# Kernel tuning notes

Measured on AMD Instinct MI355X. Metric: run time of the kernel, lower is better.

Reference implementation:

```python
import jax, jax.numpy as jnp
import numpy as np

N_NODES = 200000
N_EDGES = 800000
N_GRAPHS = 4096
IN_FEAT = 64
CONV_SIZES = [128, 128, 256, 256]
MAX_DEGREE = 5  # buckets 0..5 (degree clamped)
N_CLASSES = 2


def setup_inputs() -> dict:
    key = jax.random.key(0)
    ks = jax.random.split(key, 32)
    inp = {}
    inp["x"] = jax.random.normal(ks[0], (N_NODES, IN_FEAT), dtype=jnp.float32)
    inp["edge_index"] = jax.random.randint(ks[1], (2, N_EDGES), 0, N_NODES, dtype=jnp.int32)
    inp["batch"] = jnp.sort(jax.random.randint(ks[2], (N_NODES,), 0, N_GRAPHS, dtype=jnp.int32))
    # per-layer MFConv params: Wl (neighbor-sum branch, with bias), Wr (root branch, no bias),
    # one linear per degree bucket -> leading dim MAX_DEGREE+1
    c_in = IN_FEAT
    k = 3
    for li, c_out in enumerate(CONV_SIZES):
        s = 1.0 / np.sqrt(c_in)
        inp[f"Wl{li}"] = jax.random.normal(ks[k], (MAX_DEGREE + 1, c_in, c_out), dtype=jnp.float32) * s; k += 1
        inp[f"bl{li}"] = jax.random.normal(ks[k], (MAX_DEGREE + 1, c_out), dtype=jnp.float32) * 0.01; k += 1
        inp[f"Wr{li}"] = jax.random.normal(ks[k], (MAX_DEGREE + 1, c_in, c_out), dtype=jnp.float32) * s; k += 1
        c_in = c_out
    in_final = sum(CONV_SIZES) + CONV_SIZES[-1]  # concat of all layer outputs + pooled last layer
    inp["Wf"] = jax.random.normal(ks[k], (in_final, N_CLASSES), dtype=jnp.float32) * (1.0 / np.sqrt(in_final)); k += 1
    inp["bf"] = jax.random.normal(ks[k], (N_CLASSES,), dtype=jnp.float32) * 0.01
    return inp


def _mfconv(x, src, dst, deg, Wl, bl, Wr):
    # neighbor sum aggregation (source_to_target flow): msg_i = sum_{j->i} x_j
    msg = jax.ops.segment_sum(x[src], dst, num_segments=x.shape[0])  # [N, c_in]
    out = jnp.zeros((x.shape[0], Wl.shape[2]), dtype=x.dtype)
    for d in range(Wl.shape[0]):  # small fixed loop over degree buckets
        r = msg @ Wl[d] + bl[d] + x @ Wr[d]
        out = jnp.where((deg == d)[:, None], r, out)
    return out


def reference(x, edge_index, batch,
              Wl0, bl0, Wr0, Wl1, bl1, Wr1, Wl2, bl2, Wr2, Wl3, bl3, Wr3,
              Wf, bf):
    src, dst = edge_index[0], edge_index[1]
    n = x.shape[0]
    deg = jnp.clip(jnp.zeros((n,), jnp.int32).at[dst].add(1), 0, MAX_DEGREE)
    hs = []
    h = x
    for Wl, bl, Wr in ((Wl0, bl0, Wr0), (Wl1, bl1, Wr1), (Wl2, bl2, Wr2), (Wl3, bl3, Wr3)):
        h = _mfconv(h, src, dst, deg, Wl, bl, Wr)
        hs.append(h)
    # global_add_pool then repeat_interleave back to nodes == gather pooled by batch id
    h_pool = jax.ops.segment_sum(h, batch, num_segments=N_GRAPHS)  # [G, c_last]
    h_pool_ = h_pool[batch]  # [N, c_last]
    h_cat = jnp.concatenate(hs + [h_pool_], axis=1)  # [N, sum(sizes)+c_last]
    logits = h_cat @ Wf + bf
    return jax.nn.softmax(logits, axis=1)
```

## Files before the change

kernel.cpp:

```cpp
#include <hip/hip_runtime.h>
#include <cstdint>
#include <cstddef>

namespace {

constexpr int NN   = 200000;
constexpr int NE   = 800000;
constexpr int NG   = 4096;
constexpr int MAXD = 5;

constexpr int BM = 64;
constexpr int NBC = (NN + 255) / 256;
constexpr int NBLK  = (NN + BM - 1) / BM + 6;
constexpr int PERMN = NBLK * BM;

typedef _Float16 half8 __attribute__((ext_vector_type(8)));
typedef _Float16 half4 __attribute__((ext_vector_type(4)));
typedef float    f32x4 __attribute__((ext_vector_type(4)));

constexpr size_t P_L0 = (size_t)6 * 128 * 128;
constexpr size_t P_L1 = (size_t)6 * 256 * 128;
constexpr size_t P_L2 = (size_t)6 * 256 * 256;
constexpr size_t P_L3 = (size_t)6 * 512 * 256;
constexpr size_t O_P0 = 0;
constexpr size_t O_P1 = O_P0 + P_L0;
constexpr size_t O_P2 = O_P1 + P_L1;
constexpr size_t O_P3 = O_P2 + P_L2;
constexpr size_t WTOT = O_P3 + P_L3;


__global__ void k_memset32(int* __restrict__ p, int v, int n) {
    int i = blockIdx.x * 256 + threadIdx.x;
    if (i < n) p[i] = v;
}

__global__ void k_report(float* __restrict__ outp, float v, int n) {
    int i = blockIdx.x * 256 + threadIdx.x;
    if (i < n) outp[i] = v;
}

template <int CIN, int COUT>
__global__ void k_wpack(const float* __restrict__ Wl, const float* __restrict__ Wr,
                        _Float16* __restrict__ hi, _Float16* __restrict__ lo) {
    constexpr int NT = CIN / 16;
    constexpr int NB = COUT / 16;
    const int total = 6 * NT * NB * 64;
    int idx = blockIdx.x * 256 + threadIdx.x;
    if (idx >= total) return;
    const int lane = idx & 63;
    int rest = idx >> 6;
    const int nb = rest % NB; rest /= NB;
    const int ti = rest % NT;
    const int d  = rest / NT;
    const int k0 = ti * 32 + ((lane >> 4) * 8);
    const int n  = nb * 16 + (lane & 15);
    half8 hv, lv;
#pragma unroll
    for (int j = 0; j < 8; j++) {
        const int kk = k0 + j;
        const float v = (kk < CIN)
                            ? Wl[((size_t)d * CIN + kk) * COUT + n]
                            : Wr[((size_t)d * CIN + (kk - CIN)) * COUT + n];
        const _Float16 h = (_Float16)v;
        hv[j] = h;
        lv[j] = (_Float16)(v - (float)h);
    }
    *(half8*)(hi + (size_t)idx * 8) = hv;
    *(half8*)(lo + (size_t)idx * 8) = lv;
}


__global__ void k_count_deg(const int* __restrict__ dst, int* __restrict__ deg) {
    int e = blockIdx.x * 256 + threadIdx.x;
    if (e < NE) atomicAdd(&deg[dst[e]], 1);
}

__global__ void k_scan_part(const int* __restrict__ deg, int* __restrict__ part) {
    __shared__ int s[256];
    int t = threadIdx.x, i = blockIdx.x * 256 + t;
    s[t] = (i < NN) ? deg[i] : 0;
    __syncthreads();
    for (int st = 128; st > 0; st >>= 1) {
        if (t < st) s[t] += s[t + st];
        __syncthreads();
    }
    if (t == 0) part[blockIdx.x] = s[0];
}

__global__ void k_scan_single(int* __restrict__ part, int nb) {
    __shared__ int s[1024];
    int t = threadIdx.x;
    int v0 = (t < nb) ? part[t] : 0;
    s[t] = v0;
    __syncthreads();
    for (int off = 1; off < 1024; off <<= 1) {
        int v = (t >= off) ? s[t - off] : 0;
        __syncthreads();
        s[t] += v;
        __syncthreads();
    }
    if (t < nb) part[t] = s[t] - v0;
}

__global__ void k_scan_final(const int* __restrict__ deg, const int* __restrict__ part,
                             int* __restrict__ row_ptr, int* __restrict__ cursor) {
    __shared__ int s[256];
    int t = threadIdx.x, i = blockIdx.x * 256 + t;
    int v0 = (i < NN) ? deg[i] : 0;
    s[t] = v0;
    __syncthreads();
    for (int off = 1; off < 256; off <<= 1) {
        int v = (t >= off) ? s[t - off] : 0;
        __syncthreads();
        s[t] += v;
        __syncthreads();
    }
    if (i < NN) {
        int excl = s[t] - v0 + part[blockIdx.x];
        row_ptr[i] = excl;
        cursor[i]  = excl;
        if (i == NN - 1) row_ptr[NN] = excl + v0;
    }
}

__global__ void k_fill_csr(const int* __restrict__ src, const int* __restrict__ dst,
                           int* __restrict__ cursor, int* __restrict__ col) {
    int e = blockIdx.x * 256 + threadIdx.x;
    if (e < NE) {
        int d = dst[e];
        int slot = atomicAdd(&cursor[d], 1);
        col[slot] = src[e];
    }
}


__global__ void k_bucket_blockcount(const int* __restrict__ deg, int* __restrict__ blkcnt) {
    __shared__ int h[6];
    int t = threadIdx.x;
    if (t < 6) h[t] = 0;
    __syncthreads();
    int i = blockIdx.x * 256 + t;
    if (i < NN) atomicAdd(&h[min(deg[i], MAXD)], 1);
    __syncthreads();
    if (t < 6) blkcnt[t * NBC + blockIdx.x] = h[t];
}

__global__ void k_bucket_scanall(int* __restrict__ blkcnt, int* __restrict__ bpad) {
    __shared__ int tot[6];
    int t = threadIdx.x;
    if (t < 6) {
        int run = 0;
        for (int j = 0; j < NBC; j++) {
            int v = blkcnt[t * NBC + j];
            blkcnt[t * NBC + j] = run;
            run += v;
        }
        tot[t] = run;
    }
    __syncthreads();
    if (t == 0) {
        int off = 0;
        for (int b = 0; b < 6; b++) {
            bpad[b] = off;
            off += ((tot[b] + BM - 1) / BM) * BM;
        }
        bpad[6] = off;
    }
}

__global__ void k_scatter2(const int* __restrict__ deg, const int* __restrict__ blkcnt,
                           const int* __restrict__ bpad, int* __restrict__ perm) {
    __shared__ int base[6];
    int t = threadIdx.x;
    if (t < 6) base[t] = bpad[t] + blkcnt[t * NBC + blockIdx.x];
    __syncthreads();
    int i = blockIdx.x * 256 + t;
    if (i < NN) {
        int b = min(deg[i], MAXD);
        int pos = atomicAdd(&base[b], 1);
        perm[pos] = i;
    }
}


__global__ void k_aggregate128(const float* __restrict__ hin, const int* __restrict__ row_ptr,
                               const int* __restrict__ col, float* __restrict__ msg) {
    int node = blockIdx.x * 4 + (threadIdx.x >> 6);
    int lane = threadIdx.x & 63;
    int s = row_ptr[node], e = row_ptr[node + 1];
    float2 acc = make_float2(0.f, 0.f);
    int p = s;
    for (; p + 4 <= e; p += 4) {
        const int c0 = col[p], c1 = col[p + 1], c2 = col[p + 2], c3 = col[p + 3];
        const float2 v0 = *(const float2*)(hin + (size_t)c0 * 128 + lane * 2);
        const float2 v1 = *(const float2*)(hin + (size_t)c1 * 128 + lane * 2);
        const float2 v2 = *(const float2*)(hin + (size_t)c2 * 128 + lane * 2);
        const float2 v3 = *(const float2*)(hin + (size_t)c3 * 128 + lane * 2);
        acc.x += (v0.x + v1.x) + (v2.x + v3.x);
        acc.y += (v0.y + v1.y) + (v2.y + v3.y);
    }
    for (; p < e; p++) {
        const float2 v = *(const float2*)(hin + (size_t)col[p] * 128 + lane * 2);
        acc.x += v.x; acc.y += v.y;
    }
    *(float2*)(msg + (size_t)node * 128 + lane * 2) = acc;
}

template <int C0, int C1, int COUT, int MINW, bool POOL_FUSE>
__launch_bounds__(512, MINW)
__global__ void k_transform(const float* __restrict__ hin0, const float* __restrict__ hin1,
                            const int* __restrict__ row_ptr, const int* __restrict__ col,
                            const _Float16* __restrict__ wph, const _Float16* __restrict__ wpl,
                            const float* __restrict__ bias, const float* __restrict__ Wf,
                            const int* __restrict__ perm, const int* __restrict__ deg,
                            const int* __restrict__ batch,
                            float* __restrict__ out0, float* __restrict__ pool,
                            float* __restrict__ logits, int wf_off) {
    constexpr int CIN = C0 + C1;
    constexpr int NW  = CIN / 32;
    constexpr int NT  = 2 * NW;
    constexpr int NB  = COUT / 16;
    constexpr int NTN = NB / 8;
    constexpr int CPT = CIN / 8;
    constexpr int UQ  = CPT / 4;
    constexpr int PB_R = POOL_FUSE ? 64 : 1;
    constexpr int PB_C = 257;

    struct FragBuf {
        _Float16 Ah[NW][4][64][8];
        _Float16 Al[NW][4][64][8];
    };
    union SMemU {
        FragBuf f;
        float pbuf[PB_R][PB_C];
    };
    __shared__ SMemU sm;
    __shared__ int rowid[BM];
    __shared__ int gb[BM];
    __shared__ float lsx[BM], lsy[BM];

    const int t  = threadIdx.x;
    const int m0 = blockIdx.x * BM;

    if (t < BM) {
        rowid[t] = perm[m0 + t];
        lsx[t] = 0.f; lsy[t] = 0.f;
    }
    __syncthreads();
    if (rowid[0] < 0) return;

    const int d = min(deg[rowid[0]], MAXD);

    const int am = t & 63, aq = t >> 6;
    const int anode = rowid[am];

    if constexpr (POOL_FUSE) {
        if (t < BM) gb[t] = (rowid[t] >= 0) ? batch[rowid[t]] : -1;
    }

    {
        int es = 0, ee = 0;
        if (anode >= 0) { es = row_ptr[anode]; ee = row_ptr[anode + 1]; }
        const int k0 = CPT * aq;
        const bool lo_half = (C1 == 0) || (k0 < C0);
        const float* gsrc = lo_half ? hin0 : hin1;
        const int    gst  = lo_half ? C0 : C1;
        const int    goff = lo_half ? k0 : (k0 - C0);

        f32x4 acc1[UQ];
#pragma unroll
        for (int u = 0; u < UQ; u++) acc1[u] = (f32x4)0.f;
        for (int p = es; p < ee; p++) {
            const float* r = gsrc + (size_t)col[p] * gst + goff;
            f32x4 v[UQ];
#pragma unroll
            for (int u = 0; u < UQ; u++) v[u] = *(const f32x4*)(r + 4 * u);
#pragma unroll
            for (int u = 0; u < UQ; u++) acc1[u] += v[u];
        }
        const int mt_w = am >> 4, rl = am & 15;
#pragma unroll
        for (int u = 0; u < UQ; u++) {
            const int k  = k0 + 4 * u;
            const int ti = k >> 5;
            const int o  = (k >> 3) & 3;
            const int j0 = k & 7;
            half4 hv, lv;
#pragma unroll
            for (int i = 0; i < 4; i++) {
                const _Float16 h = (_Float16)acc1[u][i];
                hv[i] = h; lv[i] = (_Float16)(acc1[u][i] - (float)h);
            }
            *(half4*)&sm.f.Ah[ti][mt_w][rl + 16 * o][j0] = hv;
            *(half4*)&sm.f.Al[ti][mt_w][rl + 16 * o][j0] = lv;
        }
    }
    __syncthreads();

    const int lx = t & 15, qd = (t >> 4) & 3, wv = t >> 6;
    const int nb0 = wv * NTN;
    int rnode[4];
#pragma unroll
    for (int mt = 0; mt < 4; mt++) rnode[mt] = rowid[(am & 15) + 16 * mt];

    f32x4 acc[4][NTN];
#pragma unroll
    for (int mt = 0; mt < 4; mt++)
#pragma unroll
        for (int nt = 0; nt < NTN; nt++) acc[mt][nt] = (f32x4)0.f;

    for (int ti = 0; ti < NW; ti++) {
        half8 bh[NTN], bl[NTN];
        const size_t tbase = (((size_t)d * NT + ti) * NB) * 512;
#pragma unroll
        for (int nt = 0; nt < NTN; nt++) {
            const size_t off = tbase + (size_t)(nb0 + nt) * 512 + (size_t)am * 8;
            bh[nt] = *(const half8*)(wph + off);
            bl[nt] = *(const half8*)(wpl + off);
        }
        half8 ah[4], alo[4];
#pragma unroll
        for (int mt = 0; mt < 4; mt++) {
            ah[mt]  = *(const half8*)&sm.f.Ah[ti][mt][am][0];
            alo[mt] = *(const half8*)&sm.f.Al[ti][mt][am][0];
        }
#pragma unroll
        for (int nt = 0; nt < NTN; nt++)
#pragma unroll
            for (int mt = 0; mt < 4; mt++) {
                acc[mt][nt] = __builtin_amdgcn_mfma_f32_16x16x32_f16(ah[mt],  bh[nt], acc[mt][nt], 0, 0, 0);
                acc[mt][nt] = __builtin_amdgcn_mfma_f32_16x16x32_f16(alo[mt], bh[nt], acc[mt][nt], 0, 0, 0);
                acc[mt][nt] = __builtin_amdgcn_mfma_f32_16x16x32_f16(ah[mt],  bl[nt], acc[mt][nt], 0, 0, 0);
            }
    }
    for (int ti = NW; ti < NT; ti++) {
        half8 bh[NTN], bl[NTN];
        const size_t tbase = (((size_t)d * NT + ti) * NB) * 512;
#pragma unroll
        for (int nt = 0; nt < NTN; nt++) {
            const size_t off = tbase + (size_t)(nb0 + nt) * 512 + (size_t)am * 8;
            bh[nt] = *(const half8*)(wph + off);
            bl[nt] = *(const half8*)(wpl + off);
        }
        const int e = (ti - NW) * 32 + 8 * (am >> 4);
        f32x4 ra[4], rb[4];
#pragma unroll
        for (int mt = 0; mt < 4; mt++) {
            ra[mt] = (f32x4)0.f; rb[mt] = (f32x4)0.f;
            if (rnode[mt] >= 0) {
                const float* r = (C1 == 0 || e < C0)
                                     ? hin0 + (size_t)rnode[mt] * C0 + e
                                     : hin1 + (size_t)rnode[mt] * C1 + (e - C0);
                ra[mt] = *(const f32x4*)r;
                rb[mt] = *(const f32x4*)(r + 4);
            }
        }
        half8 ah[4], alo[4];
#pragma unroll
        for (int mt = 0; mt < 4; mt++) {
#pragma unroll
            for (int i = 0; i < 4; i++) {
                const _Float16 h0 = (_Float16)ra[mt][i];
                ah[mt][i] = h0;
                alo[mt][i] = (_Float16)(ra[mt][i] - (float)h0);
                const _Float16 h1 = (_Float16)rb[mt][i];
                ah[mt][4 + i] = h1;
                alo[mt][4 + i] = (_Float16)(rb[mt][i] - (float)h1);
            }
        }
#pragma unroll
        for (int nt = 0; nt < NTN; nt++)
#pragma unroll
            for (int mt = 0; mt < 4; mt++) {
                acc[mt][nt] = __builtin_amdgcn_mfma_f32_16x16x32_f16(ah[mt],  bh[nt], acc[mt][nt], 0, 0, 0);
                acc[mt][nt] = __builtin_amdgcn_mfma_f32_16x16x32_f16(alo[mt], bh[nt], acc[mt][nt], 0, 0, 0);
                acc[mt][nt] = __builtin_amdgcn_mfma_f32_16x16x32_f16(ah[mt],  bl[nt], acc[mt][nt], 0, 0, 0);
            }
    }

    float blv[NTN], w0[NTN], w1[NTN];
    int cols[NTN];
#pragma unroll
    for (int nt = 0; nt < NTN; nt++) {
        cols[nt] = wv * (16 * NTN) + nt * 16 + lx;
        blv[nt] = bias[d * COUT + cols[nt]];
        w0[nt]  = Wf[(size_t)(wf_off + cols[nt]) * 2 + 0];
        w1[nt]  = Wf[(size_t)(wf_off + cols[nt]) * 2 + 1];
    }

    __syncthreads();

#pragma unroll
    for (int mt = 0; mt < 4; mt++)
#pragma unroll
    for (int r = 0; r < 4; r++) {
        const int ri = mt * 16 + qd * 4 + r;
        const int node = rowid[ri];
        float p0 = 0.f, p1 = 0.f;
        float h[NTN];
#pragma unroll
        for (int nt = 0; nt < NTN; nt++) h[nt] = 0.f;
        if (node >= 0) {
#pragma unroll
            for (int nt = 0; nt < NTN; nt++) {
                h[nt] = acc[mt][nt][r] + blv[nt];
                p0 = fmaf(h[nt], w0[nt], p0);
                p1 = fmaf(h[nt], w1[nt], p1);
            }
            if constexpr (!POOL_FUSE) {
                float* orow = out0 + (size_t)node * COUT;
#pragma unroll
                for (int nt = 0; nt < NTN; nt++) orow[cols[nt]] = h[nt];
            }
        }
        if constexpr (POOL_FUSE) {
#pragma unroll
            for (int nt = 0; nt < NTN; nt++) sm.pbuf[ri][cols[nt]] = h[nt];
        }
#pragma unroll
        for (int s = 1; s < 16; s <<= 1) {
            p0 += __shfl_xor(p0, s, 64);
            p1 += __shfl_xor(p1, s, 64);
        }
        if (node >= 0 && lx == 0) {
            atomicAdd(&lsx[ri], p0);
            atomicAdd(&lsy[ri], p1);
        }
    }
    __syncthreads();

    if (t < BM) {
        const int node = rowid[t];
        if (node >= 0) {
            logits[(size_t)node * 2 + 0] += lsx[t];
            logits[(size_t)node * 2 + 1] += lsy[t];
        }
    }

    if constexpr (POOL_FUSE) {
        const int c  = t & 255;
        const int rh = t >> 8;
        float run = 0.f;
        int rg = -1;
        const int r0 = rh * 32, r1 = r0 + 32;
        for (int r = r0; r < r1; r++) {
            const int g = gb[r];
            if (g != rg) {
                if (rg >= 0) atomicAdd(&pool[(size_t)rg * 256 + c], run);
                run = 0.f; rg = g;
            }
            if (g >= 0) run += sm.pbuf[r][c];
        }
        if (rg >= 0) atomicAdd(&pool[(size_t)rg * 256 + c], run);
    }
}


__launch_bounds__(512, 4)
__global__ void k_gemm2b(float* __restrict__ buf0, float* __restrict__ buf1,
                         const _Float16* __restrict__ wph, const _Float16* __restrict__ wpl,
                         const float* __restrict__ bias, const float* __restrict__ Wf,
                         const int* __restrict__ perm, const int* __restrict__ deg,
                         float* __restrict__ logits) {
    constexpr int COUT = 256, NT = 8, NB = 16, NTN = 2;
    __shared__ _Float16 Ah[NT][4][64][8];
    __shared__ _Float16 Al[NT][4][64][8];
    __shared__ int rowid[BM];
    __shared__ float lsx[BM], lsy[BM];

    const int t  = threadIdx.x;
    const int m0 = blockIdx.x * BM;

    if (t < BM) {
        rowid[t] = perm[m0 + t];
        lsx[t] = 0.f; lsy[t] = 0.f;
    }
    __syncthreads();
    if (rowid[0] < 0) return;

    const int d = min(deg[rowid[0]], MAXD);

    const int am = t & 63, aq = t >> 6;
    const int anode = rowid[am];

    {
        const int k0 = 32 * aq;
        f32x4 v[8];
#pragma unroll
        for (int u = 0; u < 8; u++) v[u] = (f32x4)0.f;
        if (anode >= 0) {
            const float* r = (aq < 4) ? buf0 + (size_t)anode * 128 + k0
                                      : buf1 + (size_t)anode * 128 + (k0 - 128);
#pragma unroll
            for (int u = 0; u < 8; u++) v[u] = *(const f32x4*)(r + 4 * u);
        }
        const int mt_w = am >> 4, rl = am & 15;
#pragma unroll
        for (int u = 0; u < 8; u++) {
            const int k  = k0 + 4 * u;
            const int ti = k >> 5;
            const int o  = (k >> 3) & 3;
            const int j0 = k & 7;
            half4 hv, lv;
#pragma unroll
            for (int i = 0; i < 4; i++) {
                const _Float16 h = (_Float16)v[u][i];
                hv[i] = h; lv[i] = (_Float16)(v[u][i] - (float)h);
            }
            *(half4*)&Ah[ti][mt_w][rl + 16 * o][j0] = hv;
            *(half4*)&Al[ti][mt_w][rl + 16 * o][j0] = lv;
        }
    }
    __syncthreads();

    const int lx = t & 15, qd = (t >> 4) & 3, wv = t >> 6;
    const int nb0 = wv * NTN;

    f32x4 acc[4][NTN];
#pragma unroll
    for (int mt = 0; mt < 4; mt++)
#pragma unroll
        for (int nt = 0; nt < NTN; nt++) acc[mt][nt] = (f32x4)0.f;

    for (int ti = 0; ti < NT; ti++) {
        half8 bh[NTN], bl[NTN];
        const size_t tbase = (((size_t)d * NT + ti) * NB) * 512;
#pragma unroll
        for (int nt = 0; nt < NTN; nt++) {
            const size_t off = tbase + (size_t)(nb0 + nt) * 512 + (size_t)am * 8;
            bh[nt] = *(const half8*)(wph + off);
            bl[nt] = *(const half8*)(wpl + off);
        }
        half8 ah[4], alo[4];
#pragma unroll
        for (int mt = 0; mt < 4; mt++) {
            ah[mt]  = *(const half8*)&Ah[ti][mt][am][0];
            alo[mt] = *(const half8*)&Al[ti][mt][am][0];
        }
#pragma unroll
        for (int nt = 0; nt < NTN; nt++)
#pragma unroll
            for (int mt = 0; mt < 4; mt++) {
                acc[mt][nt] = __builtin_amdgcn_mfma_f32_16x16x32_f16(ah[mt],  bh[nt], acc[mt][nt], 0, 0, 0);
                acc[mt][nt] = __builtin_amdgcn_mfma_f32_16x16x32_f16(alo[mt], bh[nt], acc[mt][nt], 0, 0, 0);
                acc[mt][nt] = __builtin_amdgcn_mfma_f32_16x16x32_f16(ah[mt],  bl[nt], acc[mt][nt], 0, 0, 0);
            }
    }

    float blv[NTN], w0[NTN], w1[NTN];
    int cols[NTN];
#pragma unroll
    for (int nt = 0; nt < NTN; nt++) {
        cols[nt] = wv * 32 + nt * 16 + lx;
        blv[nt] = bias[d * COUT + cols[nt]];
        w0[nt]  = Wf[(size_t)(256 + cols[nt]) * 2 + 0];
        w1[nt]  = Wf[(size_t)(256 + cols[nt]) * 2 + 1];
    }
#pragma unroll
    for (int mt = 0; mt < 4; mt++)
#pragma unroll
    for (int r = 0; r < 4; r++) {
        const int ri = mt * 16 + qd * 4 + r;
        const int node = rowid[ri];
        float p0 = 0.f, p1 = 0.f;
        if (node >= 0) {
#pragma unroll
            for (int nt = 0; nt < NTN; nt++) {
                const float h = acc[mt][nt][r] + blv[nt];
                p0 = fmaf(h, w0[nt], p0);
                p1 = fmaf(h, w1[nt], p1);
                if (cols[nt] < 128) buf0[(size_t)node * 128 + cols[nt]] = h;
                else                buf1[(size_t)node * 128 + cols[nt] - 128] = h;
            }
        }
#pragma unroll
        for (int s = 1; s < 16; s <<= 1) {
            p0 += __shfl_xor(p0, s, 64);
            p1 += __shfl_xor(p1, s, 64);
        }
        if (node >= 0 && lx == 0) {
            atomicAdd(&lsx[ri], p0);
            atomicAdd(&lsy[ri], p1);
        }
    }
    __syncthreads();
    if (t < BM) {
        const int node = rowid[t];
        if (node >= 0) {
            logits[(size_t)node * 2 + 0] += lsx[t];
            logits[(size_t)node * 2 + 1] += lsy[t];
        }
    }
}


__global__ void k_pool_logits(const float* __restrict__ pool, const float* __restrict__ Wf,
                              const float* __restrict__ bf, float* __restrict__ pl) {
    int g = blockIdx.x * 4 + (threadIdx.x >> 6);
    int lane = threadIdx.x & 63;
    const float* pr = pool + (size_t)g * 256;
    float p0 = 0.f, p1 = 0.f;
#pragma unroll
    for (int j = 0; j < 4; j++) {
        int k = lane + 64 * j;
        float v = pr[k];
        p0 = fmaf(v, Wf[(size_t)(768 + k) * 2 + 0], p0);
        p1 = fmaf(v, Wf[(size_t)(768 + k) * 2 + 1], p1);
    }
#pragma unroll
    for (int s = 1; s < 64; s <<= 1) {
        p0 += __shfl_xor(p0, s, 64);
        p1 += __shfl_xor(p1, s, 64);
    }
    if (lane == 0) {
        pl[(size_t)g * 2 + 0] = p0 + bf[0];
        pl[(size_t)g * 2 + 1] = p1 + bf[1];
    }
}

__global__ void k_final(const float* __restrict__ logits, const float* __restrict__ pl,
                        const int* __restrict__ batch, float* __restrict__ outp) {
    int i = blockIdx.x * 256 + threadIdx.x;
    if (i < NN) {
        int g = batch[i];
        float l0 = logits[(size_t)i * 2 + 0] + pl[(size_t)g * 2 + 0];
        float l1 = logits[(size_t)i * 2 + 1] + pl[(size_t)g * 2 + 1];
        float m = fmaxf(l0, l1);
        float e0 = expf(l0 - m), e1 = expf(l1 - m);
        float inv = 1.f / (e0 + e1);
        outp[(size_t)i * 2 + 0] = e0 * inv;
        outp[(size_t)i * 2 + 1] = e1 * inv;
    }
}

}

extern "C" void kernel_launch(void* const* d_in, const int* in_sizes, int n_in,
                              void* d_out, int out_size, void* d_ws, size_t ws_size,
                              hipStream_t stream) {
    const float* x     = (const float*)d_in[0];
    const int*   ei    = (const int*)d_in[1];
    const int*   batch = (const int*)d_in[2];
    const float* Wl0 = (const float*)d_in[3];  const float* bl0 = (const float*)d_in[4];
    const float* Wr0 = (const float*)d_in[5];
    const float* Wl1 = (const float*)d_in[6];  const float* bl1 = (const float*)d_in[7];
    const float* Wr1 = (const float*)d_in[8];
    const float* Wl2 = (const float*)d_in[9];  const float* bl2 = (const float*)d_in[10];
    const float* Wr2 = (const float*)d_in[11];
    const float* Wl3 = (const float*)d_in[12]; const float* bl3 = (const float*)d_in[13];
    const float* Wr3 = (const float*)d_in[14];
    const float* Wf  = (const float*)d_in[15]; const float* bf  = (const float*)d_in[16];
    const int* src = ei;
    const int* dst = ei + NE;
    float* outp = (float*)d_out;
    (void)in_sizes; (void)n_in;

    char* w = (char*)d_ws;
    auto alloc = [&](size_t bytes) -> void* {
        void* p = (void*)w;
        w += (bytes + 255) & ~(size_t)255;
        return p;
    };
    int*   deg    = (int*)alloc((size_t)NN * 4);
    float* logits = (float*)alloc((size_t)NN * 2 * 4);
    float* pool   = (float*)alloc((size_t)NG * 256 * 4);
    size_t zero_words = (size_t)(w - (char*)deg) / 4;
    int*   bpad    = (int*)alloc(32);
    int*   blkcnt  = (int*)alloc((size_t)6 * NBC * 4);
    int*   perm    = (int*)alloc((size_t)PERMN * 4);
    int*   row_ptr = (int*)alloc((size_t)(NN + 1) * 4);
    int*   cursor  = (int*)alloc((size_t)NN * 4);
    int*   col     = (int*)alloc((size_t)NE * 4);
    int*   part    = (int*)alloc(1024 * 4);
    float* pl      = (float*)alloc((size_t)NG * 2 * 4);
    _Float16* whi  = (_Float16*)alloc(WTOT * 2);
    _Float16* wlo  = (_Float16*)alloc(WTOT * 2);
    float* bufA    = (float*)alloc((size_t)NN * 128 * 4);
    float* bufB    = (float*)alloc((size_t)NN * 128 * 4);

    size_t required = (size_t)(w - (char*)d_ws);
    if (required > ws_size) {
        k_report<<<(out_size + 255) / 256, 256, 0, stream>>>(
            outp, (float)(double)(ws_size >> 20), out_size);
        return;
    }

    dim3 b256(256);
    dim3 b512(512);
    k_memset32<<<(int)((zero_words + 255) / 256), b256, 0, stream>>>((int*)deg, 0, (int)zero_words);
    k_memset32<<<(PERMN + 255) / 256, b256, 0, stream>>>(perm, -1, PERMN);

    k_wpack<64, 128><<<(int)(P_L0 / 8 + 255) / 256, b256, 0, stream>>>(Wl0, Wr0, whi + O_P0, wlo + O_P0);
    k_wpack<128, 128><<<(int)(P_L1 / 8 + 255) / 256, b256, 0, stream>>>(Wl1, Wr1, whi + O_P1, wlo + O_P1);
    k_wpack<128, 256><<<(int)(P_L2 / 8 + 255) / 256, b256, 0, stream>>>(Wl2, Wr2, whi + O_P2, wlo + O_P2);
    k_wpack<256, 256><<<(int)(P_L3 / 8 + 255) / 256, b256, 0, stream>>>(Wl3, Wr3, whi + O_P3, wlo + O_P3);

    k_count_deg<<<NE / 256, b256, 0, stream>>>(dst, deg);
    k_scan_part<<<NBC, b256, 0, stream>>>(deg, part);
    k_scan_single<<<1, 1024, 0, stream>>>(part, NBC);
    k_scan_final<<<NBC, b256, 0, stream>>>(deg, part, row_ptr, cursor);
    k_fill_csr<<<NE / 256, b256, 0, stream>>>(src, dst, cursor, col);
    k_bucket_blockcount<<<NBC, b256, 0, stream>>>(deg, blkcnt);
    k_bucket_scanall<<<1, 64, 0, stream>>>(blkcnt, bpad);
    k_scatter2<<<NBC, b256, 0, stream>>>(deg, blkcnt, bpad, perm);

    k_transform<64, 0, 128, 4, false><<<dim3(NBLK), b512, 0, stream>>>(
        x, nullptr, row_ptr, col, whi + O_P0, wlo + O_P0,
        bl0, Wf, perm, deg, nullptr, bufA, nullptr, logits, 0);
    k_transform<128, 0, 128, 4, false><<<dim3(NBLK), b512, 0, stream>>>(
        bufA, nullptr, row_ptr, col, whi + O_P1, wlo + O_P1,
        bl1, Wf, perm, deg, nullptr, bufB, nullptr, logits, 128);
    k_aggregate128<<<NN / 4, b256, 0, stream>>>(bufB, row_ptr, col, bufA);
    k_gemm2b<<<dim3(NBLK), b512, 0, stream>>>(
        bufA, bufB, whi + O_P2, wlo + O_P2, bl2, Wf, perm, deg, logits);
    k_transform<128, 128, 256, 4, true><<<dim3(NBLK), b512, 0, stream>>>(
        bufA, bufB, row_ptr, col, whi + O_P3, wlo + O_P3,
        bl3, Wf, perm, deg, batch, nullptr, pool, logits, 512);

    k_pool_logits<<<NG / 4, b256, 0, stream>>>(pool, Wf, bf, pl);
    k_final<<<NBC, b256, 0, stream>>>(logits, pl, batch, outp);
}
```

Before: 1.288 ms.

## Stage root-branch features through LDS and replace shared atomics with per-wave partials

The root (x @ Wr) half of the transform kernel previously had every wave reload each node row from global memory per k-tile. It now loads those rows once cooperatively, splits them into hi/lo fp16 in shared memory (reusing the fragment buffer after a barrier), and reads them from LDS in the MFMA loop. Per-row logit partials now go into per-wave shared slots that are summed at the end, instead of shared-memory atomicAdd. The pool buffer stride also changes from 257 to 258. This adds two extra block barriers and serializes the root load after the neighbor GEMM, which may reduce load/compute overlap.

```diff
diff --git a/kernel.cpp b/kernel.cpp
--- a/kernel.cpp
+++ b/kernel.cpp
@@ -224,7 +224,7 @@
     constexpr int CPT = CIN / 8;
     constexpr int UQ  = CPT / 4;
     constexpr int PB_R = POOL_FUSE ? 64 : 1;
-    constexpr int PB_C = 257;
+    constexpr int PB_C = 258;
 
     struct FragBuf {
         _Float16 Ah[NW][4][64][8];
@@ -237,15 +237,12 @@
     __shared__ SMemU sm;
     __shared__ int rowid[BM];
     __shared__ int gb[BM];
-    __shared__ float lsx[BM], lsy[BM];
+    __shared__ float lsx[8][BM], lsy[8][BM];
 
     const int t  = threadIdx.x;
     const int m0 = blockIdx.x * BM;
 
-    if (t < BM) {
-        rowid[t] = perm[m0 + t];
-        lsx[t] = 0.f; lsy[t] = 0.f;
-    }
+    if (t < BM) rowid[t] = perm[m0 + t];
     __syncthreads();
     if (rowid[0] < 0) return;
 
@@ -258,14 +255,15 @@
         if (t < BM) gb[t] = (rowid[t] >= 0) ? batch[rowid[t]] : -1;
     }
 
+    const int k0 = CPT * aq;
+    const bool lo_half = (C1 == 0) || (k0 < C0);
+    const float* gsrc = lo_half ? hin0 : hin1;
+    const int    gst  = lo_half ? C0 : C1;
+    const int    goff = lo_half ? k0 : (k0 - C0);
+    const int mt_w = am >> 4, rl = am & 15;
     {
         int es = 0, ee = 0;
         if (anode >= 0) { es = row_ptr[anode]; ee = row_ptr[anode + 1]; }
-        const int k0 = CPT * aq;
-        const bool lo_half = (C1 == 0) || (k0 < C0);
-        const float* gsrc = lo_half ? hin0 : hin1;
-        const int    gst  = lo_half ? C0 : C1;
-        const int    goff = lo_half ? k0 : (k0 - C0);
 
         f32x4 acc1[UQ];
 #pragma unroll
@@ -278,7 +276,6 @@
 #pragma unroll
             for (int u = 0; u < UQ; u++) acc1[u] += v[u];
         }
-        const int mt_w = am >> 4, rl = am & 15;
 #pragma unroll
         for (int u = 0; u < UQ; u++) {
             const int k  = k0 + 4 * u;
@@ -299,9 +296,6 @@
 
     const int lx = t & 15, qd = (t >> 4) & 3, wv = t >> 6;
     const int nb0 = wv * NTN;
-    int rnode[4];
-#pragma unroll
-    for (int mt = 0; mt < 4; mt++) rnode[mt] = rowid[(am & 15) + 16 * mt];
 
     f32x4 acc[4][NTN];
 #pragma unroll
@@ -333,40 +327,49 @@
                 acc[mt][nt] = __builtin_amdgcn_mfma_f32_16x16x32_f16(ah[mt],  bl[nt], acc[mt][nt], 0, 0, 0);
             }
     }
-    for (int ti = NW; ti < NT; ti++) {
+    __syncthreads();
+
+    {
+        f32x4 v[UQ];
+#pragma unroll
+        for (int u = 0; u < UQ; u++) v[u] = (f32x4)0.f;
+        if (anode >= 0) {
+            const float* r = gsrc + (size_t)anode * gst + goff;
+#pragma unroll
+            for (int u = 0; u < UQ; u++) v[u] = *(const f32x4*)(r + 4 * u);
+        }
+#pragma unroll
+        for (int u = 0; u < UQ; u++) {
+            const int k  = k0 + 4 * u;
+            const int ti = k >> 5;
+            const int o  = (k >> 3) & 3;
+            const int j0 = k & 7;
+            half4 hv, lv;
+#pragma unroll
+            for (int i = 0; i < 4; i++) {
+                const _Float16 h = (_Float16)v[u][i];
+                hv[i] = h; lv[i] = (_Float16)(v[u][i] - (float)h);
+            }
+            *(half4*)&sm.f.Ah[ti][mt_w][rl + 16 * o][j0] = hv;
+            *(half4*)&sm.f.Al[ti][mt_w][rl + 16 * o][j0] = lv;
+        }
+    }
+    __syncthreads();
+
+    for (int ti = 0; ti < NW; ti++) {
         half8 bh[NTN], bl[NTN];
-        const size_t tbase = (((size_t)d * NT + ti) * NB) * 512;
+        const size_t tbase = (((size_t)d * NT + NW + ti) * NB) * 512;
 #pragma unroll
         for (int nt = 0; nt < NTN; nt++) {
             const size_t off = tbase + (size_t)(nb0 + nt) * 512 + (size_t)am * 8;
             bh[nt] = *(const half8*)(wph + off);
             bl[nt] = *(const half8*)(wpl + off);
         }
-        const int e = (ti - NW) * 32 + 8 * (am >> 4);
-        f32x4 ra[4], rb[4];
+        half8 ah[4], alo[4];
 #pragma unroll
         for (int mt = 0; mt < 4; mt++) {
-            ra[mt] = (f32x4)0.f; rb[mt] = (f32x4)0.f;
-            if (rnode[mt] >= 0) {
-                const float* r = (C1 == 0 || e < C0)
-                                     ? hin0 + (size_t)rnode[mt] * C0 + e
-                                     : hin1 + (size_t)rnode[mt] * C1 + (e - C0);
-                ra[mt] = *(const f32x4*)r;
-                rb[mt] = *(const f32x4*)(r + 4);
-            }
-        }
-        half8 ah[4], alo[4];
-#pragma unroll
-        for (int mt = 0; mt < 4; mt++) {
-#pragma unroll
-            for (int i = 0; i < 4; i++) {
-                const _Float16 h0 = (_Float16)ra[mt][i];
-                ah[mt][i] = h0;
-                alo[mt][i] = (_Float16)(ra[mt][i] - (float)h0);
-                const _Float16 h1 = (_Float16)rb[mt][i];
-                ah[mt][4 + i] = h1;
-                alo[mt][4 + i] = (_Float16)(rb[mt][i] - (float)h1);
-            }
+            ah[mt]  = *(const half8*)&sm.f.Ah[ti][mt][am][0];
+            alo[mt] = *(const half8*)&sm.f.Al[ti][mt][am][0];
         }
 #pragma unroll
         for (int nt = 0; nt < NTN; nt++)
@@ -422,9 +425,9 @@
             p0 += __shfl_xor(p0, s, 64);
             p1 += __shfl_xor(p1, s, 64);
         }
-        if (node >= 0 && lx == 0) {
-            atomicAdd(&lsx[ri], p0);
-            atomicAdd(&lsy[ri], p1);
+        if (lx == 0) {
+            lsx[wv][ri] = p0;
+            lsy[wv][ri] = p1;
         }
     }
     __syncthreads();
@@ -432,8 +435,11 @@
     if (t < BM) {
         const int node = rowid[t];
         if (node >= 0) {
-            logits[(size_t)node * 2 + 0] += lsx[t];
-            logits[(size_t)node * 2 + 1] += lsy[t];
+            float sx = 0.f, sy = 0.f;
+#pragma unroll
+            for (int w = 0; w < 8; w++) { sx += lsx[w][t]; sy += lsy[w][t]; }
+            logits[(size_t)node * 2 + 0] += sx;
+            logits[(size_t)node * 2 + 1] += sy;
         }
     }
 
@@ -466,15 +472,12 @@
     __shared__ _Float16 Ah[NT][4][64][8];
     __shared__ _Float16 Al[NT][4][64][8];
     __shared__ int rowid[BM];
-    __shared__ float lsx[BM], lsy[BM];
+    __shared__ float lsx[8][BM], lsy[8][BM];
 
     const int t  = threadIdx.x;
     const int m0 = blockIdx.x * BM;
 
-    if (t < BM) {
-        rowid[t] = perm[m0 + t];
-        lsx[t] = 0.f; lsy[t] = 0.f;
-    }
+    if (t < BM) rowid[t] = perm[m0 + t];
     __syncthreads();
     if (rowid[0] < 0) return;
 
@@ -578,17 +581,20 @@
             p0 += __shfl_xor(p0, s, 64);
             p1 += __shfl_xor(p1, s, 64);
         }
-        if (node >= 0 && lx == 0) {
-            atomicAdd(&lsx[ri], p0);
-            atomicAdd(&lsy[ri], p1);
+        if (lx == 0) {
+            lsx[wv][ri] = p0;
+            lsy[wv][ri] = p1;
         }
     }
     __syncthreads();
     if (t < BM) {
         const int node = rowid[t];
         if (node >= 0) {
-            logits[(size_t)node * 2 + 0] += lsx[t];
-            logits[(size_t)node * 2 + 1] += lsy[t];
+            float sx = 0.f, sy = 0.f;
+#pragma unroll
+            for (int w = 0; w < 8; w++) { sx += lsx[w][t]; sy += lsy[w][t]; }
+            logits[(size_t)node * 2 + 0] += sx;
+            logits[(size_t)node * 2 + 1] += sy;
         }
     }
 }
```

New measurement: 1.208 ms. 1.07x faster.
